# Optimization experiments

Measured on AMD Instinct MI355X. Metric: run time of the kernel, lower is better.

Reference implementation:

```python
import jax, jax.numpy as jnp
import numpy as np

B, HH, WW = 2, 64, 128
CX, CCONS = 117, 6
HEADS, HID = 4, 128
EDGE_DIM = 8
EMBED = 128
TGT = 39
E_EDGES = 131072
N_NODES = B * (HH * WW + 2)
LRELU = 0.01       # nn.LeakyReLU default
ATT_SLOPE = 0.2    # GATConv attention leaky slope
BN_EPS = 1e-5


def leaky(x, s=LRELU):
    return jnp.where(x >= 0, x, s * x)


def gat_conv(x, src, dst, edge_attr, W, att_src, att_dst, W_edge, att_edge, bias):
    """PyG GATConv (concat heads, add_self_loops=True, fill_value='mean')."""
    N = x.shape[0]
    E = src.shape[0]
    heads, C = att_src.shape
    # self-loop edge_attr = mean of incoming edge attrs (0 if none)
    cnt = jax.ops.segment_sum(jnp.ones((E,), x.dtype), dst, N)
    loop_attr = jax.ops.segment_sum(edge_attr, dst, N) / jnp.maximum(cnt, 1.0)[:, None]
    nodes = jnp.arange(N, dtype=src.dtype)
    s = jnp.concatenate([src, nodes])
    d = jnp.concatenate([dst, nodes])
    ea = jnp.concatenate([edge_attr, loop_attr], axis=0)
    xp = (x @ W).reshape(N, heads, C)                    # [N,h,c]
    a_src = (xp * att_src).sum(-1)                       # [N,h]
    a_dst = (xp * att_dst).sum(-1)
    ep = (ea @ W_edge).reshape(-1, heads, C)             # [E+N,h,c]
    a_edge = (ep * att_edge).sum(-1)
    alpha = leaky(a_src[s] + a_dst[d] + a_edge, ATT_SLOPE)   # [E+N,h]
    amax = jax.ops.segment_max(alpha, d, N)
    ex = jnp.exp(alpha - amax[d])
    w = ex / jax.ops.segment_sum(ex, d, N)[d]
    msg = xp[s] * w[:, :, None]                          # [E+N,h,c]
    out = jax.ops.segment_sum(msg, d, N).reshape(N, heads * C)
    return out + bias


def local_map(x):
    """Periodic longitude pad + pole rows (rolled by W/2), as construct_local_map."""
    b, c, h, w = x.shape
    mid = jnp.concatenate([x[..., -1:], x, x[..., :1]], axis=-1)            # [b,c,h,w+2]
    top = jnp.concatenate([x[:, :, 1, w // 2 - 1:], x[:, :, 1, :w // 2 + 1]], axis=-1)[:, :, None, :]
    bot = jnp.concatenate([x[:, :, -2, w // 2 - 1:], x[:, :, -2, :w // 2 + 1]], axis=-1)[:, :, None, :]
    return jnp.concatenate([top, mid, bot], axis=2)                          # [b,c,h+2,w+2]


def setup_inputs() -> dict:
    key = jax.random.key(0)
    ks = jax.random.split(key, 32)
    def nrm(i, shape, scale=0.1):
        return jax.random.normal(ks[i], shape, jnp.float32) * scale
    x = nrm(0, (B, CX, HH, WW), 1.0)
    x_cons = nrm(1, (B, CCONS, HH, WW), 1.0)
    src = jax.random.randint(ks[2], (E_EDGES,), 0, N_NODES)
    off = jax.random.randint(ks[3], (E_EDGES,), 1, N_NODES)
    dst = (src + off) % N_NODES                       # guarantees no self-loops
    edge_index = jnp.stack([src, dst]).astype(jnp.int32)
    edge_attr = nrm(4, (E_EDGES, EDGE_DIM), 1.0)
    F1 = CX + CCONS
    HC = HEADS * HID
    params = dict(
        g1_W=nrm(5, (F1, HC)), g1_as=nrm(6, (HEADS, HID)), g1_ad=nrm(7, (HEADS, HID)),
        g1_We=nrm(8, (EDGE_DIM, HC)), g1_ae=nrm(9, (HEADS, HID)), g1_b=nrm(10, (HC,)),
        g2_W=nrm(11, (HC, HC)), g2_as=nrm(12, (HEADS, HID)), g2_ad=nrm(13, (HEADS, HID)),
        g2_We=nrm(14, (EDGE_DIM, HC)), g2_ae=nrm(15, (HEADS, HID)), g2_b=nrm(16, (HC,)),
        conv_w=nrm(17, (EMBED, HC, 3, 3), 0.02), conv_b=nrm(18, (EMBED,)),
        bn_g=jnp.ones((EMBED,), jnp.float32), bn_b=jnp.zeros((EMBED,), jnp.float32),
        m_w1=nrm(19, (HC + EMBED, 512), 0.05), m_b1=nrm(20, (512,)),
        m_w2=nrm(21, (512, 256), 0.05), m_b2=nrm(22, (256,)),
        m_w3=nrm(23, (256, TGT), 0.05), m_b3=nrm(24, (TGT,)),
    )
    return dict(x=x, x_cons=x_cons, edge_index=edge_index, edge_attr=edge_attr, **params)


def _forward(x, x_cons, edge_index, edge_attr,
             g1_W, g1_as, g1_ad, g1_We, g1_ae, g1_b,
             g2_W, g2_as, g2_ad, g2_We, g2_ae, g2_b,
             conv_w, conv_b, bn_g, bn_b,
             m_w1, m_b1, m_w2, m_b2, m_w3, m_b3):
    src, dst = edge_index[0], edge_index[1]
    feats = jnp.concatenate([x, x_cons], axis=1)                 # [B,123,H,W]
    nodes = jnp.transpose(feats, (0, 2, 3, 1)).reshape(B, HH * WW, -1)
    poles = jnp.zeros((B, 2, nodes.shape[-1]), nodes.dtype)
    nodes = jnp.concatenate([poles, nodes], axis=1).reshape(B * (HH * WW + 2), -1)
    h = leaky(gat_conv(nodes, src, dst, edge_attr, g1_W, g1_as, g1_ad, g1_We, g1_ae, g1_b))
    h = leaky(gat_conv(h, src, dst, edge_attr, g2_W, g2_as, g2_ad, g2_We, g2_ae, g2_b))
    g = h.reshape(B, HH * WW + 2, -1)[:, 2:, :]                  # drop pole nodes
    gm = jnp.transpose(g.reshape(B, HH, WW, -1), (0, 3, 1, 2))   # [B,512,H,W]
    lm = local_map(gm)                                           # [B,512,H+2,W+2]
    conv = jax.lax.conv_general_dilated(lm, conv_w, (1, 1), 'VALID',
                                        dimension_numbers=('NCHW', 'OIHW', 'NCHW'))
    conv = conv + conv_b[None, :, None, None]
    # BatchNorm2d in eval mode (running_mean=0, running_var=1)
    bn = conv * (bn_g / jnp.sqrt(1.0 + BN_EPS))[None, :, None, None] + bn_b[None, :, None, None]
    nl = leaky(bn)
    nl_flat = jnp.transpose(nl, (0, 2, 3, 1)).reshape(-1, EMBED)
    xf = g.reshape(-1, HEADS * HID)
    z = jnp.concatenate([xf, nl_flat], axis=-1)                  # [B*H*W, 640]
    z = leaky(z @ m_w1 + m_b1)
    z = leaky(z @ m_w2 + m_b2)
    z = z @ m_w3 + m_b3
    delta = jnp.transpose(z.reshape(B, HH, WW, TGT), (0, 3, 1, 2))
    return delta + x[:, -TGT:]


def reference(x, x_cons, edge_index, edge_attr,
              g1_W, g1_as, g1_ad, g1_We, g1_ae, g1_b,
              g2_W, g2_as, g2_ad, g2_We, g2_ae, g2_b,
              conv_w, conv_b, bn_g, bn_b,
              m_w1, m_b1, m_w2, m_b2, m_w3, m_b3):
    return _forward(x, x_cons, edge_index, edge_attr,
                    g1_W, g1_as, g1_ad, g1_We, g1_ae, g1_b,
                    g2_W, g2_as, g2_ad, g2_We, g2_ae, g2_b,
                    conv_w, conv_b, bn_g, bn_b,
                    m_w1, m_b1, m_w2, m_b2, m_w3, m_b3)
```

## Files before the change

### kernel.cpp

```cpp
#include <hip/hip_runtime.h>
#include <math.h>
#include <type_traits>

#define NB    2
#define HHH   64
#define WWW   128
#define F1    123
#define HC    512
#define NE    131072
#define PB    8194
#define NNODE (NB*PB)
#define NPOS  (NB*HHH*WWW)
#define TGT   39
#define EMBED 128
#define KCONV 4608
#define LMROWS (2*66*130)
#define CSPLIT 3

static inline int ceildiv(int a, int b){ return (a + b - 1) / b; }

typedef short v8s __attribute__((ext_vector_type(8)));
typedef float v4f __attribute__((ext_vector_type(4)));

__device__ __forceinline__ float leakyf(float x, float s){ return x >= 0.f ? x : s * x; }

__device__ __forceinline__ unsigned short f2b(float f) {
  unsigned u = __builtin_bit_cast(unsigned, f);
  u = (u + 0x7FFFu + ((u >> 16) & 1u)) >> 16;
  return (unsigned short)u;
}
__device__ __forceinline__ float b2f(unsigned short h) {
  unsigned u = ((unsigned)h) << 16;
  return __builtin_bit_cast(float, u);
}

__device__ __forceinline__ void gload_lds16(const void* g, void* l) {
  __builtin_amdgcn_global_load_lds((const __attribute__((address_space(1))) void*)g,
                                   (__attribute__((address_space(3))) void*)l, 16, 0, 0);
}

__global__ __launch_bounds__(256) void k_build_nodes(const float* __restrict__ x,
                                                     const float* __restrict__ xc,
                                                     unsigned short* __restrict__ nodes) {
  __shared__ unsigned short lds[64][130];
  int blk = blockIdx.x;
  int b = blk >> 7, p0 = (blk & 127) * 64;
  int tid = threadIdx.x;
  int pi = tid & 63, cg = tid >> 6;
  for (int c = cg; c < 128; c += 4) {
    float v = 0.f;
    int p = p0 + pi;
    if (c < 117)      v = x[((size_t)(b * 117 + c)) * 8192 + p];
    else if (c < 123) v = xc[((size_t)(b * 6 + (c - 117))) * 8192 + p];
    lds[pi][c] = f2b(v);
  }
  if ((blk & 127) == 0 && tid < 32) {
    int rr = tid >> 4, sg = tid & 15;
    *(v8s*)(nodes + ((size_t)(b * PB + rr)) * 128 + sg * 8) = (v8s)0;
  }
  __syncthreads();
  int seg = tid & 15, r0 = tid >> 4;
  for (int rr = r0; rr < 64; rr += 16) {
    int node = b * PB + 2 + p0 + rr;
    *(v8s*)(nodes + (size_t)node * 128 + seg * 8) = *(const v8s*)(&lds[rr][seg * 8]);
  }
}

__global__ void k_hist(const int* __restrict__ dst, int* __restrict__ cnt) {
  int e = blockIdx.x * blockDim.x + threadIdx.x;
  if (e >= NE) return;
  atomicAdd(&cnt[dst[e]], 1);
}

__global__ void k_scan(const int* __restrict__ cnt, int* __restrict__ rowptr, int n) {
  __shared__ int part[512];
  int t = threadIdx.x;
  int chunk = (n + 511) >> 9;
  int beg = t * chunk, end = min(beg + chunk, n);
  int s = 0;
  for (int i = beg; i < end; i++) s += cnt[i];
  part[t] = s;
  __syncthreads();
  int own = s;
  for (int off = 1; off < 512; off <<= 1) {
    int v = 0;
    if (t >= off) v = part[t - off];
    __syncthreads();
    part[t] += v;
    __syncthreads();
  }
  int run = part[t] - own;
  for (int i = beg; i < end; i++) { rowptr[i] = run; run += cnt[i]; }
  if (t == 511) rowptr[n] = part[511];
}

__global__ void k_copy_int(const int* __restrict__ a, int* __restrict__ b, int n) {
  int i = blockIdx.x * blockDim.x + threadIdx.x;
  if (i < n) b[i] = a[i];
}

__global__ void k_scatter(const int* __restrict__ dst, int* __restrict__ cursor,
                          int* __restrict__ colidx) {
  int e = blockIdx.x * blockDim.x + threadIdx.x;
  if (e >= NE) return;
  int pos = atomicAdd(&cursor[dst[e]], 1);
  colidx[pos] = e;
}

__global__ void k_loop_attr(const float* __restrict__ eattr, const int* __restrict__ rowptr,
                            const int* __restrict__ colidx, float* __restrict__ lattr) {
  int idx = blockIdx.x * blockDim.x + threadIdx.x;
  if (idx >= NNODE * 8) return;
  int nn = idx >> 3, k = idx & 7;
  int b = rowptr[nn], e = rowptr[nn + 1];
  float s = 0.f;
  for (int i = b; i < e; i++) s += eattr[(size_t)colidx[i] * 8 + k];
  int c = e - b;
  lattr[idx] = s / (float)max(c, 1);
}

__global__ void k_medge(const float* __restrict__ We, const float* __restrict__ ae,
                        float* __restrict__ M) {
  int t = threadIdx.x;
  if (t >= 32) return;
  int k = t >> 2, h = t & 3;
  float s = 0.f;
  for (int c = 0; c < 128; c++) s += We[k * 512 + h * 128 + c] * ae[h * 128 + c];
  M[t] = s;
}

__global__ void k_aedge(const float* __restrict__ attr, const float* __restrict__ M,
                        float* __restrict__ out, int n) {
  int idx = blockIdx.x * blockDim.x + threadIdx.x;
  if (idx >= n * 4) return;
  int e = idx >> 2, h = idx & 3;
  float s = 0.f;
#pragma unroll
  for (int k = 0; k < 8; k++) s += attr[(size_t)e * 8 + k] * M[k * 4 + h];
  out[idx] = s;
}

__global__ void k_attn_dots(const unsigned short* __restrict__ xp, const float* __restrict__ as,
                            const float* __restrict__ ad, float* __restrict__ a_src,
                            float* __restrict__ a_dst) {
  int gw = (blockIdx.x * blockDim.x + threadIdx.x) >> 6;
  int lane = threadIdx.x & 63;
  if (gw >= NNODE) return;
  int h = lane >> 4;
  int c0 = (lane & 15) * 8;
  v8s v = *(const v8s*)(xp + (size_t)gw * HC + h * 128 + c0);
  const float* asr = as + h * 128 + c0;
  const float* adr = ad + h * 128 + c0;
  float s1 = 0.f, s2 = 0.f;
#pragma unroll
  for (int i = 0; i < 8; i++) {
    float f = b2f((unsigned short)v[i]);
    s1 += f * asr[i]; s2 += f * adr[i];
  }
  for (int off = 1; off < 16; off <<= 1) { s1 += __shfl_xor(s1, off); s2 += __shfl_xor(s2, off); }
  if ((lane & 15) == 0) { a_src[gw * 4 + h] = s1; a_dst[gw * 4 + h] = s2; }
}

__global__ __launch_bounds__(256) void k_aggregate(
    const unsigned short* __restrict__ xp, const float* __restrict__ a_src,
    const float* __restrict__ a_dst, const float* __restrict__ a_edge,
    const float* __restrict__ a_eloop, const int* __restrict__ srcv,
    const int* __restrict__ rowptr, const int* __restrict__ colidx,
    const float* __restrict__ bias, unsigned short* __restrict__ outp,
    int ldo, int pole) {
  int n = blockIdx.x;
  int tid = threadIdx.x;
  int wid = tid >> 6, lane = tid & 63;
  __shared__ float sh_w[64][4];
  __shared__ int   sh_s[64];
  __shared__ float sh_m[4], sh_l[4], sh_r[4];
  __shared__ float pacc[4][512];
  if (pole) {
    int b = n / PB, loc = n - b * PB;
    if (loc < 2) return;
    outp += (size_t)(b * 8192 + loc - 2) * ldo;
  } else {
    outp += (size_t)n * ldo;
  }
  int beg = rowptr[n], deg = rowptr[n + 1] - beg;
  int total = deg + 1;
  if (tid < 4) { sh_m[tid] = -1e30f; sh_l[tid] = 0.f; }
  float acc[8] = {0.f, 0.f, 0.f, 0.f, 0.f, 0.f, 0.f, 0.f};
  int c0 = lane * 8;
  int hh = lane >> 4;
  float adn = a_dst[(size_t)n * 4 + (tid & 3)];
  __syncthreads();
  for (int base = 0; base < total; base += 64) {
    int cnt = min(64, total - base);
    if (tid < cnt * 4) {
      int le = tid >> 2, h = tid & 3;
      int ge = base + le;
      int sn; float ae;
      if (ge < deg) { int eid = colidx[beg + ge]; sn = srcv[eid]; ae = a_edge[(size_t)eid * 4 + h]; }
      else          { sn = n; ae = a_eloop[(size_t)n * 4 + h]; }
      float al = a_src[(size_t)sn * 4 + h] + adn + ae;
      sh_w[le][h] = leakyf(al, 0.2f);
      if (h == 0) sh_s[le] = sn;
    }
    __syncthreads();
    {
      int h = wid;
      float a = (lane < cnt) ? sh_w[lane][h] : -1e30f;
      float cm = a;
#pragma unroll
      for (int off = 1; off < 64; off <<= 1) cm = fmaxf(cm, __shfl_xor(cm, off));
      float m_old = sh_m[h];
      float nm = fmaxf(m_old, cm);
      float ex = (lane < cnt) ? __expf(a - nm) : 0.f;
      float s = ex;
#pragma unroll
      for (int off = 1; off < 64; off <<= 1) s += __shfl_xor(s, off);
      if (lane < cnt) sh_w[lane][h] = ex;
      if (lane == 0) {
        float r = __expf(m_old - nm);
        sh_r[h] = r; sh_m[h] = nm; sh_l[h] = sh_l[h] * r + s;
      }
    }
    __syncthreads();
    float r = sh_r[hh];
#pragma unroll
    for (int j = 0; j < 8; j++) acc[j] *= r;
    for (int e = wid; e < cnt; e += 4) {
      int sn = sh_s[e];
      float wt = sh_w[e][hh];
      v8s v = *(const v8s*)(xp + (size_t)sn * HC + c0);
#pragma unroll
      for (int j = 0; j < 8; j++) acc[j] += wt * b2f((unsigned short)v[j]);
    }
    __syncthreads();
  }
  *(v4f*)(&pacc[wid][c0])     = *(const v4f*)(&acc[0]);
  *(v4f*)(&pacc[wid][c0 + 4]) = *(const v4f*)(&acc[4]);
  __syncthreads();
  int c = tid * 2;
  float l = sh_l[c >> 7];
  float v0 = (pacc[0][c] + pacc[1][c] + pacc[2][c] + pacc[3][c]) / l + bias[c];
  float v1 = (pacc[0][c+1] + pacc[1][c+1] + pacc[2][c+1] + pacc[3][c+1]) / l + bias[c+1];
  unsigned o = (unsigned)f2b(leakyf(v0, 0.01f)) | ((unsigned)f2b(leakyf(v1, 0.01f)) << 16);
  *(unsigned*)(outp + c) = o;
}

__global__ void k_bt(const float* __restrict__ src, unsigned short* __restrict__ bt,
                     int N, int Ks, int Kd) {
  int idx = blockIdx.x * blockDim.x + threadIdx.x;
  if (idx >= N * Kd) return;
  int n = idx / Kd, k = idx - n * Kd;
  bt[idx] = (k < Ks) ? f2b(src[(size_t)k * N + n]) : (unsigned short)0;
}

__global__ void k_convbt(const float* __restrict__ w, unsigned short* __restrict__ bt) {
  int idx = blockIdx.x * blockDim.x + threadIdx.x;
  if (idx >= EMBED * KCONV) return;
  int n = idx / KCONV, k = idx - n * KCONV;
  int tap = k >> 9, c = k & 511;
  bt[idx] = f2b(w[(size_t)n * KCONV + c * 9 + tap]);
}

__global__ void k_lm(const unsigned short* __restrict__ zin, unsigned short* __restrict__ lmb) {
  int idx = blockIdx.x * blockDim.x + threadIdx.x;
  if (idx >= LMROWS * 64) return;
  int c8 = (idx & 63) * 8;
  int prow = idx >> 6;
  int cc = prow % 130;
  int t = prow / 130;
  int rr = t % 66, b = t / 66;
  int gr, gc;
  if (rr == 0)       { gr = 1;      gc = (63 + cc) & 127; }
  else if (rr == 65) { gr = 62;     gc = (63 + cc) & 127; }
  else               { gr = rr - 1; gc = (cc + 127) & 127; }
  *(v8s*)(lmb + (size_t)prow * 512 + c8) =
      *(const v8s*)(zin + ((size_t)(b * 8192 + gr * WWW + gc)) * 640 + c8);
}

template<int MODE, int BM, int BN, typename OutT>
__global__ __launch_bounds__(256) void mgemm(
    int M, int N, int K, int ldb,
    const unsigned short* __restrict__ A, int lda,
    const unsigned short* __restrict__ Bt,
    const float* __restrict__ bias,
    const float* __restrict__ bnscale, const float* __restrict__ bnshift,
    float slope,
    OutT* __restrict__ C, int ldc)
{
  constexpr int WM = BM / 32;
  constexpr int WN = BN / 32;
  constexpr int ACH = BM * 4;
  constexpr int BCH = BN * 4;
  __shared__ unsigned short As[2][BM * 32];
  __shared__ unsigned short Bs[2][BN * 32];
  int tid = threadIdx.x;
  int wid = tid >> 6, lane = tid & 63;
  int wr = wid >> 1, wc = wid & 1;
  int l15 = lane & 15, l4 = lane >> 4;
  int slot8 = (l4 ^ (l15 & 3)) * 8;
  int row0 = blockIdx.y * BM;
  int col0, koff;
  if constexpr (MODE == 2) { col0 = 0; koff = blockIdx.x * K; C += (size_t)blockIdx.x * M * ldc; }
  else { col0 = blockIdx.x * BN; koff = 0; }

  auto stage = [&](int buf, int kt) {
    int k0 = kt * 32;
    int kg = koff + k0;
    int di = 0, dj = 0;
    if constexpr (MODE >= 1) { int tap = kg >> 9; di = tap / 3; dj = tap - di * 3; }
#pragma unroll
    for (int i = 0; i < ACH / 256; i++) {
      int c = i * 256 + tid;
      int r = c >> 2;
      int seg = (c & 3) ^ (r & 3);
      const unsigned short* ga;
      if constexpr (MODE == 0) {
        int gr = min(row0 + r, M - 1);
        ga = A + (size_t)gr * lda + k0 + seg * 8;
      } else {
        int gr = row0 + r;
        int b = gr >> 13, pos = gr & 8191, ii = pos >> 7, jj = pos & 127;
        int arow = (b * 66 + ii + di) * 130 + (jj + dj);
        ga = A + (size_t)arow * 512 + (kg & 511) + seg * 8;
      }
      gload_lds16(ga, &As[buf][c * 8]);
    }
#pragma unroll
    for (int i = 0; i < BCH / 256; i++) {
      int c = i * 256 + tid;
      int r = c >> 2;
      int seg = (c & 3) ^ (r & 3);
      int gn = min(col0 + r, N - 1);
      gload_lds16(Bt + (size_t)gn * ldb + kg + seg * 8, &Bs[buf][c * 8]);
    }
  };

  v4f acc[WM][WN];
#pragma unroll
  for (int m = 0; m < WM; m++)
#pragma unroll
    for (int n = 0; n < WN; n++) acc[m][n] = (v4f)0.f;

  int nt = K >> 5;
  stage(0, 0);
  __syncthreads();
  int cur = 0;
  for (int t = 0; t < nt - 1; t++) {
    stage(cur ^ 1, t + 1);
    v8s a[WM], b[WN];
#pragma unroll
    for (int m = 0; m < WM; m++)
      a[m] = *(const v8s*)(&As[cur][(wr * (BM / 2) + m * 16 + l15) * 32 + slot8]);
#pragma unroll
    for (int n = 0; n < WN; n++)
      b[n] = *(const v8s*)(&Bs[cur][(wc * (BN / 2) + n * 16 + l15) * 32 + slot8]);
#pragma unroll
    for (int m = 0; m < WM; m++)
#pragma unroll
      for (int n = 0; n < WN; n++)
        acc[m][n] = __builtin_amdgcn_mfma_f32_16x16x32_bf16(a[m], b[n], acc[m][n], 0, 0, 0);
    __syncthreads();
    cur ^= 1;
  }
  {
    v8s a[WM], b[WN];
#pragma unroll
    for (int m = 0; m < WM; m++)
      a[m] = *(const v8s*)(&As[cur][(wr * (BM / 2) + m * 16 + l15) * 32 + slot8]);
#pragma unroll
    for (int n = 0; n < WN; n++)
      b[n] = *(const v8s*)(&Bs[cur][(wc * (BN / 2) + n * 16 + l15) * 32 + slot8]);
#pragma unroll
    for (int m = 0; m < WM; m++)
#pragma unroll
      for (int n = 0; n < WN; n++)
        acc[m][n] = __builtin_amdgcn_mfma_f32_16x16x32_bf16(a[m], b[n], acc[m][n], 0, 0, 0);
  }
#pragma unroll
  for (int m = 0; m < WM; m++) {
#pragma unroll
    for (int q = 0; q < 4; q++) {
      int r = row0 + wr * (BM / 2) + m * 16 + l4 * 4 + q;
      if (r >= M) continue;
#pragma unroll
      for (int n = 0; n < WN; n++) {
        int cc = col0 + wc * (BN / 2) + n * 16 + l15;
        if (cc >= N) continue;
        float v = acc[m][n][q];
        if constexpr (MODE != 2) {
          if (bias) v += bias[cc];
          if (bnscale) v = v * (bnscale[cc] * rsqrtf(1.f + 1e-5f)) + bnshift[cc];
          v = leakyf(v, slope);
        }
        if constexpr (std::is_same<OutT, float>::value) {
          C[(size_t)r * ldc + cc] = v;
        } else {
          C[(size_t)r * ldc + cc] = f2b(v);
        }
      }
    }
  }
}

__global__ void k_creduce(const float* __restrict__ p, const float* __restrict__ convb,
                          const float* __restrict__ bng, const float* __restrict__ bnb,
                          unsigned short* __restrict__ zin) {
  int idx = blockIdx.x * blockDim.x + threadIdx.x;
  if (idx >= NPOS * 32) return;
  int r = idx >> 5, c4 = (idx & 31) * 4;
  const float4* p0 = (const float4*)(p + (size_t)r * 128 + c4);
  const float4* p1 = (const float4*)(p + (size_t)(NPOS + r) * 128 + c4);
  const float4* p2 = (const float4*)(p + (size_t)(2 * NPOS + r) * 128 + c4);
  float4 a = *p0, b = *p1, c = *p2;
  unsigned short* o = zin + (size_t)r * 640 + 512 + c4;
#pragma unroll
  for (int j = 0; j < 4; j++) {
    float v = ((const float*)&a)[j] + ((const float*)&b)[j] + ((const float*)&c)[j];
    int cc = c4 + j;
    v += convb[cc];
    v = v * (bng[cc] * rsqrtf(1.f + 1e-5f)) + bnb[cc];
    o[j] = f2b(leakyf(v, 0.01f));
  }
}

__global__ void k_final(const float* __restrict__ z3, const float* __restrict__ x,
                        float* __restrict__ outp) {
  int idx = blockIdx.x * blockDim.x + threadIdx.x;
  if (idx >= NPOS * TGT) return;
  int b = idx / (TGT * 8192);
  int rem = idx - b * (TGT * 8192);
  int t = rem >> 13;
  int p = rem & 8191;
  outp[idx] = z3[((size_t)(b * 8192 + p)) * TGT + t] + x[((size_t)(b * 117 + 78 + t)) * 8192 + p];
}

extern "C" void kernel_launch(void* const* d_in, const int* in_sizes, int n_in,
                              void* d_out, int out_size, void* d_ws, size_t ws_size,
                              hipStream_t stream) {
  const float* x     = (const float*)d_in[0];
  const float* xcons = (const float*)d_in[1];
  const int*   eidx  = (const int*)d_in[2];
  const float* eattr = (const float*)d_in[3];
  const float* g1W  = (const float*)d_in[4];
  const float* g1as = (const float*)d_in[5];
  const float* g1ad = (const float*)d_in[6];
  const float* g1We = (const float*)d_in[7];
  const float* g1ae = (const float*)d_in[8];
  const float* g1b  = (const float*)d_in[9];
  const float* g2W  = (const float*)d_in[10];
  const float* g2as = (const float*)d_in[11];
  const float* g2ad = (const float*)d_in[12];
  const float* g2We = (const float*)d_in[13];
  const float* g2ae = (const float*)d_in[14];
  const float* g2b  = (const float*)d_in[15];
  const float* convw= (const float*)d_in[16];
  const float* convb= (const float*)d_in[17];
  const float* bng  = (const float*)d_in[18];
  const float* bnb  = (const float*)d_in[19];
  const float* mw1  = (const float*)d_in[20];
  const float* mb1  = (const float*)d_in[21];
  const float* mw2  = (const float*)d_in[22];
  const float* mb2  = (const float*)d_in[23];
  const float* mw3  = (const float*)d_in[24];
  const float* mb3  = (const float*)d_in[25];
  float* outp = (float*)d_out;
  (void)in_sizes; (void)n_in; (void)out_size; (void)ws_size;

  const int* esrc = eidx;
  const int* edst = eidx + NE;

  char* basep = (char*)d_ws;
  size_t off = 0;
  auto alloc = [&](size_t bytes) -> void* {
    void* p = basep + off;
    off += (bytes + 255) & ~(size_t)255;
    return p;
  };
  unsigned short* nodesb = (unsigned short*)alloc((size_t)NNODE * 128 * 2);
  unsigned short* xpb    = (unsigned short*)alloc((size_t)NNODE * HC * 2);
  unsigned short* h1b    = (unsigned short*)alloc((size_t)NNODE * HC * 2);
  unsigned short* lmb    = (unsigned short*)alloc((size_t)LMROWS * 512 * 2);
  unsigned short* zin    = (unsigned short*)alloc((size_t)NPOS * 640 * 2);
  float* cpart  = (float*)alloc((size_t)CSPLIT * NPOS * 128 * sizeof(float));
  float* asrc   = (float*)alloc((size_t)NNODE * 4 * sizeof(float));
  float* adst   = (float*)alloc((size_t)NNODE * 4 * sizeof(float));
  float* aedge  = (float*)alloc((size_t)NE * 4 * sizeof(float));
  float* aeloop = (float*)alloc((size_t)NNODE * 4 * sizeof(float));
  float* lattr  = (float*)alloc((size_t)NNODE * 8 * sizeof(float));
  float* Medge  = (float*)alloc(32 * sizeof(float));
  unsigned short* g1Wt  = (unsigned short*)alloc((size_t)512 * 128 * 2);
  unsigned short* g2Wt  = (unsigned short*)alloc((size_t)512 * 512 * 2);
  unsigned short* convWt= (unsigned short*)alloc((size_t)EMBED * KCONV * 2);
  unsigned short* mw1t  = (unsigned short*)alloc((size_t)512 * 640 * 2);
  unsigned short* mw2t  = (unsigned short*)alloc((size_t)256 * 512 * 2);
  unsigned short* mw3t  = (unsigned short*)alloc((size_t)TGT * 256 * 2);
  int* cnt      = (int*)alloc((size_t)NNODE * sizeof(int));
  int* rowptr   = (int*)alloc((size_t)(NNODE + 1) * sizeof(int));
  int* cursor   = (int*)alloc((size_t)NNODE * sizeof(int));
  int* colidx   = (int*)alloc((size_t)NE * sizeof(int));
  unsigned short* z1b = xpb;
  unsigned short* z2b = h1b;
  float*          z3  = (float*)nodesb;

  hipMemsetAsync(cnt, 0, NNODE * sizeof(int), stream);
  k_build_nodes<<<NB * 128, 256, 0, stream>>>(x, xcons, nodesb);
  k_hist<<<ceildiv(NE, 256), 256, 0, stream>>>(edst, cnt);
  k_scan<<<1, 512, 0, stream>>>(cnt, rowptr, NNODE);
  k_copy_int<<<ceildiv(NNODE, 256), 256, 0, stream>>>(rowptr, cursor, NNODE);
  k_scatter<<<ceildiv(NE, 256), 256, 0, stream>>>(edst, cursor, colidx);
  k_loop_attr<<<ceildiv(NNODE * 8, 256), 256, 0, stream>>>(eattr, rowptr, colidx, lattr);

  k_bt<<<ceildiv(512 * 128, 256), 256, 0, stream>>>(g1W, g1Wt, 512, F1, 128);
  k_bt<<<ceildiv(512 * 512, 256), 256, 0, stream>>>(g2W, g2Wt, 512, 512, 512);
  k_convbt<<<ceildiv(EMBED * KCONV, 256), 256, 0, stream>>>(convw, convWt);
  k_bt<<<ceildiv(512 * 640, 256), 256, 0, stream>>>(mw1, mw1t, 512, 640, 640);
  k_bt<<<ceildiv(256 * 512, 256), 256, 0, stream>>>(mw2, mw2t, 256, 512, 512);
  k_bt<<<ceildiv(TGT * 256, 256), 256, 0, stream>>>(mw3, mw3t, TGT, 256, 256);

  k_medge<<<1, 64, 0, stream>>>(g1We, g1ae, Medge);
  k_aedge<<<ceildiv(NE * 4, 256), 256, 0, stream>>>(eattr, Medge, aedge, NE);
  k_aedge<<<ceildiv(NNODE * 4, 256), 256, 0, stream>>>(lattr, Medge, aeloop, NNODE);
  {
    dim3 g(4, ceildiv(NNODE, 128));
    mgemm<0, 128, 128, unsigned short><<<g, 256, 0, stream>>>(
        NNODE, HC, 128, 128, nodesb, 128, g1Wt, nullptr, nullptr, nullptr, 1.0f, xpb, HC);
  }
  k_attn_dots<<<ceildiv(NNODE, 4), 256, 0, stream>>>(xpb, g1as, g1ad, asrc, adst);
  k_aggregate<<<NNODE, 256, 0, stream>>>(xpb, asrc, adst, aedge, aeloop, esrc, rowptr,
                                         colidx, g1b, h1b, HC, 0);

  k_medge<<<1, 64, 0, stream>>>(g2We, g2ae, Medge);
  k_aedge<<<ceildiv(NE * 4, 256), 256, 0, stream>>>(eattr, Medge, aedge, NE);
  k_aedge<<<ceildiv(NNODE * 4, 256), 256, 0, stream>>>(lattr, Medge, aeloop, NNODE);
  {
    dim3 g(4, ceildiv(NNODE, 128));
    mgemm<0, 128, 128, unsigned short><<<g, 256, 0, stream>>>(
        NNODE, HC, HC, HC, h1b, HC, g2Wt, nullptr, nullptr, nullptr, 1.0f, xpb, HC);
  }
  k_attn_dots<<<ceildiv(NNODE, 4), 256, 0, stream>>>(xpb, g2as, g2ad, asrc, adst);
  k_aggregate<<<NNODE, 256, 0, stream>>>(xpb, asrc, adst, aedge, aeloop, esrc, rowptr,
                                         colidx, g2b, zin, 640, 1);

  k_lm<<<ceildiv(LMROWS * 64, 256), 256, 0, stream>>>(zin, lmb);
  {
    dim3 g(CSPLIT, ceildiv(NPOS, 64));
    mgemm<2, 64, 128, float><<<g, 256, 0, stream>>>(
        NPOS, EMBED, KCONV / CSPLIT, KCONV, lmb, 512, convWt,
        nullptr, nullptr, nullptr, 1.0f, cpart, EMBED);
  }
  k_creduce<<<ceildiv(NPOS * 32, 256), 256, 0, stream>>>(cpart, convb, bng, bnb, zin);

  {
    dim3 g(4, ceildiv(NPOS, 128));
    mgemm<0, 128, 128, unsigned short><<<g, 256, 0, stream>>>(
        NPOS, 512, 640, 640, zin, 640, mw1t, mb1, nullptr, nullptr, 0.01f, z1b, 512);
  }
  {
    dim3 g(2, ceildiv(NPOS, 64));
    mgemm<0, 64, 128, unsigned short><<<g, 256, 0, stream>>>(
        NPOS, 256, 512, 512, z1b, 512, mw2t, mb2, nullptr, nullptr, 0.01f, z2b, 256);
  }
  {
    dim3 g(1, ceildiv(NPOS, 64));
    mgemm<0, 64, 64, float><<<g, 256, 0, stream>>>(
        NPOS, TGT, 256, 256, z2b, 256, mw3t, mb3, nullptr, nullptr, 1.0f, z3, TGT);
  }

  k_final<<<ceildiv(NPOS * TGT, 256), 256, 0, stream>>>(z3, x, outp);
}
```

Before: 349.9 us.

## Restructure conv as per-tap GEMM plus tap-sum; one wave per node aggregation

The 3x3 conv is reformulated: one GEMM computes per-pixel projections for all 9 taps (N=1152) from the unpadded features, and a new tap-sum kernel gathers the shifted tap outputs with the pole/periodic mapping and applies bias, batch norm and leaky ReLU. This removes the local-map materialization, the split-K partial buffer and the reduce kernel, but stores the 9x intermediate in bf16. Separately, GAT aggregation now uses one wavefront per node with shuffles instead of a 256-thread block with shared memory and barriers. The LDS swizzle in the GEMM is also dropped, which may introduce bank conflicts.

New measurement: 331.0 us. -5.4%, faster.

```diff
diff --git a/kernel.cpp b/kernel.cpp
--- a/kernel.cpp
+++ b/kernel.cpp
@@ -14,8 +14,7 @@
 #define TGT   39
 #define EMBED 128
 #define KCONV 4608
-#define LMROWS (2*66*130)
-#define CSPLIT 3
+#define NTAPK 1152
 
 static inline int ceildiv(int a, int b){ return (a + b - 1) / b; }
 
@@ -168,13 +167,9 @@
     const int* __restrict__ rowptr, const int* __restrict__ colidx,
     const float* __restrict__ bias, unsigned short* __restrict__ outp,
     int ldo, int pole) {
-  int n = blockIdx.x;
-  int tid = threadIdx.x;
-  int wid = tid >> 6, lane = tid & 63;
-  __shared__ float sh_w[64][4];
-  __shared__ int   sh_s[64];
-  __shared__ float sh_m[4], sh_l[4], sh_r[4];
-  __shared__ float pacc[4][512];
+  int wid = threadIdx.x >> 6, lane = threadIdx.x & 63;
+  int n = blockIdx.x * 4 + wid;
+  if (n >= NNODE) return;
   if (pole) {
     int b = n / PB, loc = n - b * PB;
     if (loc < 2) return;
@@ -184,65 +179,63 @@
   }
   int beg = rowptr[n], deg = rowptr[n + 1] - beg;
   int total = deg + 1;
-  if (tid < 4) { sh_m[tid] = -1e30f; sh_l[tid] = 0.f; }
+  int ha = lane & 3;
+  int ea = lane >> 2;
+  int hh = lane >> 4;
+  int c0 = lane * 8;
+  float adn = a_dst[(size_t)n * 4 + ha];
+  float m0 = -1e30f, m1 = -1e30f, m2 = -1e30f, m3 = -1e30f;
+  float l0 = 0.f, l1 = 0.f, l2 = 0.f, l3 = 0.f;
   float acc[8] = {0.f, 0.f, 0.f, 0.f, 0.f, 0.f, 0.f, 0.f};
-  int c0 = lane * 8;
-  int hh = lane >> 4;
-  float adn = a_dst[(size_t)n * 4 + (tid & 3)];
-  __syncthreads();
-  for (int base = 0; base < total; base += 64) {
-    int cnt = min(64, total - base);
-    if (tid < cnt * 4) {
-      int le = tid >> 2, h = tid & 3;
-      int ge = base + le;
-      int sn; float ae;
-      if (ge < deg) { int eid = colidx[beg + ge]; sn = srcv[eid]; ae = a_edge[(size_t)eid * 4 + h]; }
-      else          { sn = n; ae = a_eloop[(size_t)n * 4 + h]; }
-      float al = a_src[(size_t)sn * 4 + h] + adn + ae;
-      sh_w[le][h] = leakyf(al, 0.2f);
-      if (h == 0) sh_s[le] = sn;
+  for (int base = 0; base < total; base += 16) {
+    int cnt = min(16, total - base);
+    int ge = base + ea;
+    int sn = n;
+    float al = -1e30f;
+    if (ea < cnt) {
+      float aev;
+      if (ge < deg) { int eid = colidx[beg + ge]; sn = srcv[eid]; aev = a_edge[(size_t)eid * 4 + ha]; }
+      else          { aev = a_eloop[(size_t)n * 4 + ha]; }
+      al = leakyf(a_src[(size_t)sn * 4 + ha] + adn + aev, 0.2f);
     }
-    __syncthreads();
-    {
-      int h = wid;
-      float a = (lane < cnt) ? sh_w[lane][h] : -1e30f;
-      float cm = a;
-#pragma unroll
-      for (int off = 1; off < 64; off <<= 1) cm = fmaxf(cm, __shfl_xor(cm, off));
-      float m_old = sh_m[h];
-      float nm = fmaxf(m_old, cm);
-      float ex = (lane < cnt) ? __expf(a - nm) : 0.f;
-      float s = ex;
-#pragma unroll
-      for (int off = 1; off < 64; off <<= 1) s += __shfl_xor(s, off);
-      if (lane < cnt) sh_w[lane][h] = ex;
-      if (lane == 0) {
-        float r = __expf(m_old - nm);
-        sh_r[h] = r; sh_m[h] = nm; sh_l[h] = sh_l[h] * r + s;
-      }
-    }
-    __syncthreads();
-    float r = sh_r[hh];
-#pragma unroll
-    for (int j = 0; j < 8; j++) acc[j] *= r;
-    for (int e = wid; e < cnt; e += 4) {
-      int sn = sh_s[e];
-      float wt = sh_w[e][hh];
-      v8s v = *(const v8s*)(xp + (size_t)sn * HC + c0);
+    float cm = al;
+    cm = fmaxf(cm, __shfl_xor(cm, 4));
+    cm = fmaxf(cm, __shfl_xor(cm, 8));
+    cm = fmaxf(cm, __shfl_xor(cm, 16));
+    cm = fmaxf(cm, __shfl_xor(cm, 32));
+    float cm0 = __shfl(cm, 0), cm1 = __shfl(cm, 1), cm2 = __shfl(cm, 2), cm3 = __shfl(cm, 3);
+    float nm0 = fmaxf(m0, cm0), nm1 = fmaxf(m1, cm1), nm2 = fmaxf(m2, cm2), nm3 = fmaxf(m3, cm3);
+    float r0 = __expf(m0 - nm0), r1 = __expf(m1 - nm1), r2 = __expf(m2 - nm2), r3 = __expf(m3 - nm3);
+    float nmh = ha == 0 ? nm0 : ha == 1 ? nm1 : ha == 2 ? nm2 : nm3;
+    float ex = (ea < cnt) ? __expf(al - nmh) : 0.f;
+    float s = ex;
+    s += __shfl_xor(s, 4);
+    s += __shfl_xor(s, 8);
+    s += __shfl_xor(s, 16);
+    s += __shfl_xor(s, 32);
+    float s0 = __shfl(s, 0), s1 = __shfl(s, 1), s2 = __shfl(s, 2), s3 = __shfl(s, 3);
+    l0 = l0 * r0 + s0; l1 = l1 * r1 + s1; l2 = l2 * r2 + s2; l3 = l3 * r3 + s3;
+    m0 = nm0; m1 = nm1; m2 = nm2; m3 = nm3;
+    float rh = hh == 0 ? r0 : hh == 1 ? r1 : hh == 2 ? r2 : r3;
+#pragma unroll
+    for (int j = 0; j < 8; j++) acc[j] *= rh;
+    for (int e = 0; e < cnt; e++) {
+      float wt = __shfl(ex, e * 4 + hh);
+      int se = __shfl(sn, e * 4);
+      v8s v = *(const v8s*)(xp + (size_t)se * HC + c0);
 #pragma unroll
       for (int j = 0; j < 8; j++) acc[j] += wt * b2f((unsigned short)v[j]);
     }
-    __syncthreads();
-  }
-  *(v4f*)(&pacc[wid][c0])     = *(const v4f*)(&acc[0]);
-  *(v4f*)(&pacc[wid][c0 + 4]) = *(const v4f*)(&acc[4]);
-  __syncthreads();
-  int c = tid * 2;
-  float l = sh_l[c >> 7];
-  float v0 = (pacc[0][c] + pacc[1][c] + pacc[2][c] + pacc[3][c]) / l + bias[c];
-  float v1 = (pacc[0][c+1] + pacc[1][c+1] + pacc[2][c+1] + pacc[3][c+1]) / l + bias[c+1];
-  unsigned o = (unsigned)f2b(leakyf(v0, 0.01f)) | ((unsigned)f2b(leakyf(v1, 0.01f)) << 16);
-  *(unsigned*)(outp + c) = o;
+  }
+  float lh = hh == 0 ? l0 : hh == 1 ? l1 : hh == 2 ? l2 : l3;
+  float inv = 1.f / lh;
+  v8s o;
+#pragma unroll
+  for (int j = 0; j < 8; j++) {
+    float v = acc[j] * inv + bias[c0 + j];
+    o[j] = (short)f2b(leakyf(v, 0.01f));
+  }
+  *(v8s*)(outp + c0) = o;
 }
 
 __global__ void k_bt(const float* __restrict__ src, unsigned short* __restrict__ bt,
@@ -255,35 +248,18 @@
 
 __global__ void k_convbt(const float* __restrict__ w, unsigned short* __restrict__ bt) {
   int idx = blockIdx.x * blockDim.x + threadIdx.x;
-  if (idx >= EMBED * KCONV) return;
-  int n = idx / KCONV, k = idx - n * KCONV;
-  int tap = k >> 9, c = k & 511;
-  bt[idx] = f2b(w[(size_t)n * KCONV + c * 9 + tap]);
-}
-
-__global__ void k_lm(const unsigned short* __restrict__ zin, unsigned short* __restrict__ lmb) {
-  int idx = blockIdx.x * blockDim.x + threadIdx.x;
-  if (idx >= LMROWS * 64) return;
-  int c8 = (idx & 63) * 8;
-  int prow = idx >> 6;
-  int cc = prow % 130;
-  int t = prow / 130;
-  int rr = t % 66, b = t / 66;
-  int gr, gc;
-  if (rr == 0)       { gr = 1;      gc = (63 + cc) & 127; }
-  else if (rr == 65) { gr = 62;     gc = (63 + cc) & 127; }
-  else               { gr = rr - 1; gc = (cc + 127) & 127; }
-  *(v8s*)(lmb + (size_t)prow * 512 + c8) =
-      *(const v8s*)(zin + ((size_t)(b * 8192 + gr * WWW + gc)) * 640 + c8);
-}
-
-template<int MODE, int BM, int BN, typename OutT>
+  if (idx >= NTAPK * 512) return;
+  int j = idx >> 9, c = idx & 511;
+  int tap = j >> 7, nn = j & 127;
+  bt[idx] = f2b(w[(size_t)nn * KCONV + c * 9 + tap]);
+}
+
+template<int BM, int BN, typename OutT>
 __global__ __launch_bounds__(256) void mgemm(
     int M, int N, int K, int ldb,
     const unsigned short* __restrict__ A, int lda,
     const unsigned short* __restrict__ Bt,
     const float* __restrict__ bias,
-    const float* __restrict__ bnscale, const float* __restrict__ bnshift,
     float slope,
     OutT* __restrict__ C, int ldc)
 {
@@ -297,41 +273,24 @@
   int wid = tid >> 6, lane = tid & 63;
   int wr = wid >> 1, wc = wid & 1;
   int l15 = lane & 15, l4 = lane >> 4;
-  int slot8 = (l4 ^ (l15 & 3)) * 8;
   int row0 = blockIdx.y * BM;
-  int col0, koff;
-  if constexpr (MODE == 2) { col0 = 0; koff = blockIdx.x * K; C += (size_t)blockIdx.x * M * ldc; }
-  else { col0 = blockIdx.x * BN; koff = 0; }
+  int col0 = blockIdx.x * BN;
 
   auto stage = [&](int buf, int kt) {
     int k0 = kt * 32;
-    int kg = koff + k0;
-    int di = 0, dj = 0;
-    if constexpr (MODE >= 1) { int tap = kg >> 9; di = tap / 3; dj = tap - di * 3; }
 #pragma unroll
     for (int i = 0; i < ACH / 256; i++) {
       int c = i * 256 + tid;
-      int r = c >> 2;
-      int seg = (c & 3) ^ (r & 3);
-      const unsigned short* ga;
-      if constexpr (MODE == 0) {
-        int gr = min(row0 + r, M - 1);
-        ga = A + (size_t)gr * lda + k0 + seg * 8;
-      } else {
-        int gr = row0 + r;
-        int b = gr >> 13, pos = gr & 8191, ii = pos >> 7, jj = pos & 127;
-        int arow = (b * 66 + ii + di) * 130 + (jj + dj);
-        ga = A + (size_t)arow * 512 + (kg & 511) + seg * 8;
-      }
-      gload_lds16(ga, &As[buf][c * 8]);
+      int r = c >> 2, seg = c & 3;
+      int gr = min(row0 + r, M - 1);
+      gload_lds16(A + (size_t)gr * lda + k0 + seg * 8, &As[buf][c * 8]);
     }
 #pragma unroll
     for (int i = 0; i < BCH / 256; i++) {
       int c = i * 256 + tid;
-      int r = c >> 2;
-      int seg = (c & 3) ^ (r & 3);
+      int r = c >> 2, seg = c & 3;
       int gn = min(col0 + r, N - 1);
-      gload_lds16(Bt + (size_t)gn * ldb + kg + seg * 8, &Bs[buf][c * 8]);
+      gload_lds16(Bt + (size_t)gn * ldb + k0 + seg * 8, &Bs[buf][c * 8]);
     }
   };
 
@@ -350,10 +309,10 @@
     v8s a[WM], b[WN];
 #pragma unroll
     for (int m = 0; m < WM; m++)
-      a[m] = *(const v8s*)(&As[cur][(wr * (BM / 2) + m * 16 + l15) * 32 + slot8]);
+      a[m] = *(const v8s*)(&As[cur][(wr * (BM / 2) + m * 16 + l15) * 32 + l4 * 8]);
 #pragma unroll
     for (int n = 0; n < WN; n++)
-      b[n] = *(const v8s*)(&Bs[cur][(wc * (BN / 2) + n * 16 + l15) * 32 + slot8]);
+      b[n] = *(const v8s*)(&Bs[cur][(wc * (BN / 2) + n * 16 + l15) * 32 + l4 * 8]);
 #pragma unroll
     for (int m = 0; m < WM; m++)
 #pragma unroll
@@ -366,10 +325,10 @@
     v8s a[WM], b[WN];
 #pragma unroll
     for (int m = 0; m < WM; m++)
-      a[m] = *(const v8s*)(&As[cur][(wr * (BM / 2) + m * 16 + l15) * 32 + slot8]);
+      a[m] = *(const v8s*)(&As[cur][(wr * (BM / 2) + m * 16 + l15) * 32 + l4 * 8]);
 #pragma unroll
     for (int n = 0; n < WN; n++)
-      b[n] = *(const v8s*)(&Bs[cur][(wc * (BN / 2) + n * 16 + l15) * 32 + slot8]);
+      b[n] = *(const v8s*)(&Bs[cur][(wc * (BN / 2) + n * 16 + l15) * 32 + l4 * 8]);
 #pragma unroll
     for (int m = 0; m < WM; m++)
 #pragma unroll
@@ -387,11 +346,8 @@
         int cc = col0 + wc * (BN / 2) + n * 16 + l15;
         if (cc >= N) continue;
         float v = acc[m][n][q];
-        if constexpr (MODE != 2) {
-          if (bias) v += bias[cc];
-          if (bnscale) v = v * (bnscale[cc] * rsqrtf(1.f + 1e-5f)) + bnshift[cc];
-          v = leakyf(v, slope);
-        }
+        if (bias) v += bias[cc];
+        v = leakyf(v, slope);
         if constexpr (std::is_same<OutT, float>::value) {
           C[(size_t)r * ldc + cc] = v;
         } else {
@@ -402,25 +358,37 @@
   }
 }
 
-__global__ void k_creduce(const float* __restrict__ p, const float* __restrict__ convb,
-                          const float* __restrict__ bng, const float* __restrict__ bnb,
-                          unsigned short* __restrict__ zin) {
+__global__ void k_tapsum(const unsigned short* __restrict__ H,
+                         const float* __restrict__ convb, const float* __restrict__ bng,
+                         const float* __restrict__ bnb, unsigned short* __restrict__ zin) {
   int idx = blockIdx.x * blockDim.x + threadIdx.x;
-  if (idx >= NPOS * 32) return;
-  int r = idx >> 5, c4 = (idx & 31) * 4;
-  const float4* p0 = (const float4*)(p + (size_t)r * 128 + c4);
-  const float4* p1 = (const float4*)(p + (size_t)(NPOS + r) * 128 + c4);
-  const float4* p2 = (const float4*)(p + (size_t)(2 * NPOS + r) * 128 + c4);
-  float4 a = *p0, b = *p1, c = *p2;
-  unsigned short* o = zin + (size_t)r * 640 + 512 + c4;
-#pragma unroll
-  for (int j = 0; j < 4; j++) {
-    float v = ((const float*)&a)[j] + ((const float*)&b)[j] + ((const float*)&c)[j];
-    int cc = c4 + j;
-    v += convb[cc];
+  if (idx >= NPOS * 16) return;
+  int r = idx >> 4, seg = idx & 15;
+  int n0 = seg * 8;
+  int b = r >> 13, pos = r & 8191, i = pos >> 7, j = pos & 127;
+  float acc[8] = {0.f, 0.f, 0.f, 0.f, 0.f, 0.f, 0.f, 0.f};
+#pragma unroll
+  for (int tap = 0; tap < 9; tap++) {
+    int di = tap / 3, dj = tap - di * 3;
+    int rr = i + di, cc = j + dj;
+    int gr, gc;
+    if (rr == 0)       { gr = 1;      gc = (63 + cc) & 127; }
+    else if (rr == 65) { gr = 62;     gc = (63 + cc) & 127; }
+    else               { gr = rr - 1; gc = (cc + 127) & 127; }
+    v8s v = *(const v8s*)(H + ((size_t)(b * 8192 + gr * WWW + gc)) * NTAPK + tap * 128 + n0);
+#pragma unroll
+    for (int q = 0; q < 8; q++) acc[q] += b2f((unsigned short)v[q]);
+  }
+  unsigned short* o = zin + (size_t)r * 640 + 512 + n0;
+  v8s ov;
+#pragma unroll
+  for (int q = 0; q < 8; q++) {
+    int cc = n0 + q;
+    float v = acc[q] + convb[cc];
     v = v * (bng[cc] * rsqrtf(1.f + 1e-5f)) + bnb[cc];
-    o[j] = f2b(leakyf(v, 0.01f));
-  }
+    ov[q] = (short)f2b(leakyf(v, 0.01f));
+  }
+  *(v8s*)o = ov;
 }
 
 __global__ void k_final(const float* __restrict__ z3, const float* __restrict__ x,
@@ -479,9 +447,8 @@
   unsigned short* nodesb = (unsigned short*)alloc((size_t)NNODE * 128 * 2);
   unsigned short* xpb    = (unsigned short*)alloc((size_t)NNODE * HC * 2);
   unsigned short* h1b    = (unsigned short*)alloc((size_t)NNODE * HC * 2);
-  unsigned short* lmb    = (unsigned short*)alloc((size_t)LMROWS * 512 * 2);
   unsigned short* zin    = (unsigned short*)alloc((size_t)NPOS * 640 * 2);
-  float* cpart  = (float*)alloc((size_t)CSPLIT * NPOS * 128 * sizeof(float));
+  unsigned short* Hb     = (unsigned short*)alloc((size_t)NPOS * NTAPK * 2);
   float* asrc   = (float*)alloc((size_t)NNODE * 4 * sizeof(float));
   float* adst   = (float*)alloc((size_t)NNODE * 4 * sizeof(float));
   float* aedge  = (float*)alloc((size_t)NE * 4 * sizeof(float));
@@ -490,7 +457,7 @@
   float* Medge  = (float*)alloc(32 * sizeof(float));
   unsigned short* g1Wt  = (unsigned short*)alloc((size_t)512 * 128 * 2);
   unsigned short* g2Wt  = (unsigned short*)alloc((size_t)512 * 512 * 2);
-  unsigned short* convWt= (unsigned short*)alloc((size_t)EMBED * KCONV * 2);
+  unsigned short* convWt= (unsigned short*)alloc((size_t)NTAPK * 512 * 2);
   unsigned short* mw1t  = (unsigned short*)alloc((size_t)512 * 640 * 2);
   unsigned short* mw2t  = (unsigned short*)alloc((size_t)256 * 512 * 2);
   unsigned short* mw3t  = (unsigned short*)alloc((size_t)TGT * 256 * 2);
@@ -512,7 +479,7 @@
 
   k_bt<<<ceildiv(512 * 128, 256), 256, 0, stream>>>(g1W, g1Wt, 512, F1, 128);
   k_bt<<<ceildiv(512 * 512, 256), 256, 0, stream>>>(g2W, g2Wt, 512, 512, 512);
-  k_convbt<<<ceildiv(EMBED * KCONV, 256), 256, 0, stream>>>(convw, convWt);
+  k_convbt<<<ceildiv(NTAPK * 512, 256), 256, 0, stream>>>(convw, convWt);
   k_bt<<<ceildiv(512 * 640, 256), 256, 0, stream>>>(mw1, mw1t, 512, 640, 640);
   k_bt<<<ceildiv(256 * 512, 256), 256, 0, stream>>>(mw2, mw2t, 256, 512, 512);
   k_bt<<<ceildiv(TGT * 256, 256), 256, 0, stream>>>(mw3, mw3t, TGT, 256, 256);
@@ -522,48 +489,46 @@
   k_aedge<<<ceildiv(NNODE * 4, 256), 256, 0, stream>>>(lattr, Medge, aeloop, NNODE);
   {
     dim3 g(4, ceildiv(NNODE, 128));
-    mgemm<0, 128, 128, unsigned short><<<g, 256, 0, stream>>>(
-        NNODE, HC, 128, 128, nodesb, 128, g1Wt, nullptr, nullptr, nullptr, 1.0f, xpb, HC);
+    mgemm<128, 128, unsigned short><<<g, 256, 0, stream>>>(
+        NNODE, HC, 128, 128, nodesb, 128, g1Wt, nullptr, 1.0f, xpb, HC);
   }
   k_attn_dots<<<ceildiv(NNODE, 4), 256, 0, stream>>>(xpb, g1as, g1ad, asrc, adst);
-  k_aggregate<<<NNODE, 256, 0, stream>>>(xpb, asrc, adst, aedge, aeloop, esrc, rowptr,
-                                         colidx, g1b, h1b, HC, 0);
+  k_aggregate<<<ceildiv(NNODE, 4), 256, 0, stream>>>(xpb, asrc, adst, aedge, aeloop, esrc,
+                                                     rowptr, colidx, g1b, h1b, HC, 0);
 
   k_medge<<<1, 64, 0, stream>>>(g2We, g2ae, Medge);
   k_aedge<<<ceildiv(NE * 4, 256), 256, 0, stream>>>(eattr, Medge, aedge, NE);
   k_aedge<<<ceildiv(NNODE * 4, 256), 256, 0, stream>>>(lattr, Medge, aeloop, NNODE);
   {
     dim3 g(4, ceildiv(NNODE, 128));
-    mgemm<0, 128, 128, unsigned short><<<g, 256, 0, stream>>>(
-        NNODE, HC, HC, HC, h1b, HC, g2Wt, nullptr, nullptr, nullptr, 1.0f, xpb, HC);
+    mgemm<128, 128, unsigned short><<<g, 256, 0, stream>>>(
+        NNODE, HC, HC, HC, h1b, HC, g2Wt, nullptr, 1.0f, xpb, HC);
   }
   k_attn_dots<<<ceildiv(NNODE, 4), 256, 0, stream>>>(xpb, g2as, g2ad, asrc, adst);
-  k_aggregate<<<NNODE, 256, 0, stream>>>(xpb, asrc, adst, aedge, aeloop, esrc, rowptr,
-                                         colidx, g2b, zin, 640, 1);
-
-  k_lm<<<ceildiv(LMROWS * 64, 256), 256, 0, stream>>>(zin, lmb);
-  {
-    dim3 g(CSPLIT, ceildiv(NPOS, 64));
-    mgemm<2, 64, 128, float><<<g, 256, 0, stream>>>(
-        NPOS, EMBED, KCONV / CSPLIT, KCONV, lmb, 512, convWt,
-        nullptr, nullptr, nullptr, 1.0f, cpart, EMBED);
-  }
-  k_creduce<<<ceildiv(NPOS * 32, 256), 256, 0, stream>>>(cpart, convb, bng, bnb, zin);
+  k_aggregate<<<ceildiv(NNODE, 4), 256, 0, stream>>>(xpb, asrc, adst, aedge, aeloop, esrc,
+                                                     rowptr, colidx, g2b, zin, 640, 1);
+
+  {
+    dim3 g(NTAPK / 128, ceildiv(NPOS, 128));
+    mgemm<128, 128, unsigned short><<<g, 256, 0, stream>>>(
+        NPOS, NTAPK, 512, 512, zin, 640, convWt, nullptr, 1.0f, Hb, NTAPK);
+  }
+  k_tapsum<<<ceildiv(NPOS * 16, 256), 256, 0, stream>>>(Hb, convb, bng, bnb, zin);
 
   {
     dim3 g(4, ceildiv(NPOS, 128));
-    mgemm<0, 128, 128, unsigned short><<<g, 256, 0, stream>>>(
-        NPOS, 512, 640, 640, zin, 640, mw1t, mb1, nullptr, nullptr, 0.01f, z1b, 512);
+    mgemm<128, 128, unsigned short><<<g, 256, 0, stream>>>(
+        NPOS, 512, 640, 640, zin, 640, mw1t, mb1, 0.01f, z1b, 512);
   }
   {
     dim3 g(2, ceildiv(NPOS, 64));
-    mgemm<0, 64, 128, unsigned short><<<g, 256, 0, stream>>>(
-        NPOS, 256, 512, 512, z1b, 512, mw2t, mb2, nullptr, nullptr, 0.01f, z2b, 256);
+    mgemm<64, 128, unsigned short><<<g, 256, 0, stream>>>(
+        NPOS, 256, 512, 512, z1b, 512, mw2t, mb2, 0.01f, z2b, 256);
   }
   {
     dim3 g(1, ceildiv(NPOS, 64));
-    mgemm<0, 64, 64, float><<<g, 256, 0, stream>>>(
-        NPOS, TGT, 256, 256, z2b, 256, mw3t, mb3, nullptr, nullptr, 1.0f, z3, TGT);
+    mgemm<64, 64, float><<<g, 256, 0, stream>>>(
+        NPOS, TGT, 256, 256, z2b, 256, mw3t, mb3, 1.0f, z3, TGT);
   }
 
   k_final<<<ceildiv(NPOS * TGT, 256), 256, 0, stream>>>(z3, x, outp);
```
